# Optimization experiments

Hardware: AMD Instinct MI355X
Metric: run time of the kernel (lower is better)

Reference implementation:

```python
import jax, jax.numpy as jnp
import numpy as np

LAMBDA_COORD = 5.0
LAMBDA_NOOBJ = 0.5
EPS = 1e-9


def _bbox_iou(px, py, pr, gx, gy, gr):
    """IoU of the axis-aligned bounding squares of two circles (x, y, r)."""
    l1, r1, t1, b1 = px - pr, px + pr, py - pr, py + pr
    l2, r2, t2, b2 = gx - gr, gx + gr, gy - gr, gy + gr
    iw = jnp.maximum(jnp.minimum(r1, r2) - jnp.maximum(l1, l2), 0.0)
    ih = jnp.maximum(jnp.minimum(b1, b2) - jnp.maximum(t1, t2), 0.0)
    inter = iw * ih
    a1 = (r1 - l1) * (b1 - t1)
    a2 = (r2 - l2) * (b2 - t2)
    return inter / (a1 + a2 - inter + EPS)


def setup_inputs() -> dict:
    key = jax.random.key(0)
    k1, k2, k3, k4 = jax.random.split(key, 4)
    B, L, G, C = 65536, 16, 8, 8
    pred = jax.random.uniform(k1, (B, G, G, C), dtype=jnp.float32)
    label_rc = jax.random.randint(k2, (B, L, 2), 0, G, dtype=jnp.int32)
    xy = jax.random.uniform(k3, (B, L, 2), dtype=jnp.float32)
    r = jax.random.uniform(k4, (B, L, 1), dtype=jnp.float32) * 0.2 + 0.01
    label_box = jnp.concatenate([xy, r], axis=-1)
    return {"pred": pred, "label_rc": label_rc, "label_box": label_box}


def reference(pred, label_rc, label_box):
    B = pred.shape[0]
    rows = label_rc[..., 0]  # [B, L]
    cols = label_rc[..., 1]
    bidx = jnp.arange(B)[:, None]
    pb = pred[bidx, rows, cols]  # [B, L, 8] responsible cell per label

    gx, gy, gr = label_box[..., 0], label_box[..., 1], label_box[..., 2]
    iou1 = _bbox_iou(pb[..., 0], pb[..., 1], pb[..., 2], gx, gy, gr)
    iou2 = _bbox_iou(pb[..., 4], pb[..., 5], pb[..., 6], gx, gy, gr)

    swap = iou2 > iou1
    cx = jnp.where(swap, pb[..., 4], pb[..., 0])
    cy = jnp.where(swap, pb[..., 5], pb[..., 1])
    cr = jnp.where(swap, pb[..., 6], pb[..., 2])
    conf = jnp.where(swap, pb[..., 7], pb[..., 3])
    un_conf = jnp.where(swap, pb[..., 3], pb[..., 7])
    bigger = jnp.where(swap, iou2, iou1)
    smaller = jnp.where(swap, iou1, iou2)

    coord_loss = LAMBDA_COORD * jnp.sum(
        (cx - gx) ** 2 + (cy - gy) ** 2 + (cr - gr) ** 2)
    cond_loss = jnp.sum((bigger - conf) ** 2)
    cond_loss = cond_loss + LAMBDA_NOOBJ * jnp.sum((smaller - un_conf) ** 2)

    # object mask over the 8x8 grid (duplicates collapse to 1, as in original)
    obj_mask = jnp.zeros(pred.shape[:3], dtype=pred.dtype).at[bidx, rows, cols].set(1.0)
    noobj = (pred[..., 3] ** 2 + pred[..., 7] ** 2) * (1.0 - obj_mask)
    cond_loss = cond_loss + LAMBDA_NOOBJ * jnp.sum(noobj)

    return (coord_loss + cond_loss) / B
```

## Files before the change

kernel.cpp:

```cpp
#include <hip/hip_runtime.h>


static constexpr float LAMBDA_COORD = 5.0f;
static constexpr float LAMBDA_NOOBJ = 0.5f;
static constexpr float EPS_F = 1e-9f;

__device__ __forceinline__ float bbox_iou(float px, float py, float pr,
                                          float gx, float gy, float gr) {
    float l1 = px - pr, r1 = px + pr, t1 = py - pr, b1 = py + pr;
    float l2 = gx - gr, r2 = gx + gr, t2 = gy - gr, b2 = gy + gr;
    float iw = fmaxf(fminf(r1, r2) - fmaxf(l1, l2), 0.0f);
    float ih = fmaxf(fminf(b1, b2) - fmaxf(t1, t2), 0.0f);
    float inter = iw * ih;
    float a1 = (r1 - l1) * (b1 - t1);
    float a2 = (r2 - l2) * (b2 - t2);
    return inter / (a1 + a2 - inter + EPS_F);
}

__global__ void zero_out_kernel(float* __restrict__ out) { *out = 0.0f; }

__global__ __launch_bounds__(256) void yolo_loss_kernel(
    const float* __restrict__ pred,
    const int*   __restrict__ label_rc,
    const float* __restrict__ label_box,
    float* __restrict__ out,
    int B, int L, float invB)
{
    const int lane    = threadIdx.x & 63;
    const int wave_ib = threadIdx.x >> 6;
    const int wave    = blockIdx.x * (blockDim.x >> 6) + wave_ib;
    const int nwaves  = gridDim.x * (blockDim.x >> 6);

    float acc = 0.0f;

    for (int b = wave; b < B; b += nwaves) {
        const float* cell_ptr = pred + ((size_t)b << 9) + ((size_t)lane << 3);
        float4 q0 = *(const float4*)(cell_ptr);
        float4 q1 = *(const float4*)(cell_ptr + 4);

        int   cell = -1;
        float gx = 0.f, gy = 0.f, gr = 0.f;
        if (lane < L) {
            const int2 rc = *(const int2*)(label_rc + ((size_t)b * L + lane) * 2);
            cell = rc.x * 8 + rc.y;
            const float* lb = label_box + ((size_t)b * L + lane) * 3;
            gx = lb[0]; gy = lb[1]; gr = lb[2];
        }

        bool labeled = false;
        #pragma unroll
        for (int l = 0; l < 16; ++l) {
            if (l < L) labeled |= (__shfl(cell, l) == lane);
        }

        int src = (cell < 0) ? 0 : cell;
        float p0 = __shfl(q0.x, src);
        float p1 = __shfl(q0.y, src);
        float p2 = __shfl(q0.z, src);
        float p3 = __shfl(q0.w, src);
        float p4 = __shfl(q1.x, src);
        float p5 = __shfl(q1.y, src);
        float p6 = __shfl(q1.z, src);
        float p7 = __shfl(q1.w, src);

        float contrib = labeled ? 0.0f
                      : LAMBDA_NOOBJ * (q0.w * q0.w + q1.w * q1.w);

        if (lane < L) {
            float iou1 = bbox_iou(p0, p1, p2, gx, gy, gr);
            float iou2 = bbox_iou(p4, p5, p6, gx, gy, gr);
            bool  sw   = iou2 > iou1;
            float cx      = sw ? p4 : p0;
            float cy      = sw ? p5 : p1;
            float cr      = sw ? p6 : p2;
            float conf    = sw ? p7 : p3;
            float un_conf = sw ? p3 : p7;
            float bigger  = sw ? iou2 : iou1;
            float smaller = sw ? iou1 : iou2;
            float dx = cx - gx, dy = cy - gy, dr = cr - gr;
            contrib += LAMBDA_COORD * (dx * dx + dy * dy + dr * dr);
            float d1 = bigger - conf;
            float d2 = smaller - un_conf;
            contrib += d1 * d1 + LAMBDA_NOOBJ * (d2 * d2);
        }

        acc += contrib;
    }

    #pragma unroll
    for (int off = 32; off > 0; off >>= 1)
        acc += __shfl_xor(acc, off);

    __shared__ float wsum[4];
    if (lane == 0) wsum[wave_ib] = acc;
    __syncthreads();
    if (threadIdx.x == 0) {
        float s = wsum[0] + wsum[1] + wsum[2] + wsum[3];
        atomicAdd(out, s * invB);
    }
}

extern "C" void kernel_launch(void* const* d_in, const int* in_sizes, int n_in,
                              void* d_out, int out_size, void* d_ws, size_t ws_size,
                              hipStream_t stream) {
    const float* pred      = (const float*)d_in[0];
    const int*   label_rc  = (const int*)d_in[1];
    const float* label_box = (const float*)d_in[2];
    float*       out       = (float*)d_out;

    const int B = in_sizes[0] / 512;
    const int L = in_sizes[1] / (B * 2);
    const float invB = 1.0f / (float)B;

    zero_out_kernel<<<1, 1, 0, stream>>>(out);

    const int threads = 256;
    const int blocks  = 1024;
    yolo_loss_kernel<<<blocks, threads, 0, stream>>>(
        pred, label_rc, label_box, out, B, L, invB);
}
```

Before: 210.3 us.

## Launch one wave per batch item and replace atomics with two-pass reduction

```diff
diff --git a/kernel.cpp b/kernel.cpp
--- a/kernel.cpp
+++ b/kernel.cpp
@@ -17,23 +17,20 @@
     return inter / (a1 + a2 - inter + EPS_F);
 }
 
-__global__ void zero_out_kernel(float* __restrict__ out) { *out = 0.0f; }
-
 __global__ __launch_bounds__(256) void yolo_loss_kernel(
     const float* __restrict__ pred,
     const int*   __restrict__ label_rc,
     const float* __restrict__ label_box,
-    float* __restrict__ out,
-    int B, int L, float invB)
+    float* __restrict__ partials,
+    int B, int L)
 {
     const int lane    = threadIdx.x & 63;
     const int wave_ib = threadIdx.x >> 6;
-    const int wave    = blockIdx.x * (blockDim.x >> 6) + wave_ib;
-    const int nwaves  = gridDim.x * (blockDim.x >> 6);
+    const int b       = blockIdx.x * 4 + wave_ib;
 
-    float acc = 0.0f;
+    float contrib = 0.0f;
 
-    for (int b = wave; b < B; b += nwaves) {
+    if (b < B) {
         const float* cell_ptr = pred + ((size_t)b << 9) + ((size_t)lane << 3);
         float4 q0 = *(const float4*)(cell_ptr);
         float4 q1 = *(const float4*)(cell_ptr + 4);
@@ -63,8 +60,8 @@
         float p6 = __shfl(q1.z, src);
         float p7 = __shfl(q1.w, src);
 
-        float contrib = labeled ? 0.0f
-                      : LAMBDA_NOOBJ * (q0.w * q0.w + q1.w * q1.w);
+        contrib = labeled ? 0.0f
+                : LAMBDA_NOOBJ * (q0.w * q0.w + q1.w * q1.w);
 
         if (lane < L) {
             float iou1 = bbox_iou(p0, p1, p2, gx, gy, gr);
@@ -83,21 +80,40 @@
             float d2 = smaller - un_conf;
             contrib += d1 * d1 + LAMBDA_NOOBJ * (d2 * d2);
         }
-
-        acc += contrib;
     }
 
     #pragma unroll
     for (int off = 32; off > 0; off >>= 1)
-        acc += __shfl_xor(acc, off);
+        contrib += __shfl_xor(contrib, off);
 
     __shared__ float wsum[4];
-    if (lane == 0) wsum[wave_ib] = acc;
+    if (lane == 0) wsum[wave_ib] = contrib;
     __syncthreads();
-    if (threadIdx.x == 0) {
-        float s = wsum[0] + wsum[1] + wsum[2] + wsum[3];
-        atomicAdd(out, s * invB);
+    if (threadIdx.x == 0)
+        partials[blockIdx.x] = wsum[0] + wsum[1] + wsum[2] + wsum[3];
+}
+
+__global__ __launch_bounds__(256) void reduce_kernel(
+    const float* __restrict__ partials, float* __restrict__ out,
+    int n4, float invB)
+{
+    const float4* p4 = (const float4*)partials;
+    float4 s4 = make_float4(0.f, 0.f, 0.f, 0.f);
+    for (int i = threadIdx.x; i < n4; i += 256) {
+        float4 v = p4[i];
+        s4.x += v.x; s4.y += v.y; s4.z += v.z; s4.w += v.w;
     }
+    float s = (s4.x + s4.y) + (s4.z + s4.w);
+    #pragma unroll
+    for (int off = 32; off > 0; off >>= 1)
+        s += __shfl_xor(s, off);
+
+    __shared__ float wsum[4];
+    const int lane = threadIdx.x & 63, w = threadIdx.x >> 6;
+    if (lane == 0) wsum[w] = s;
+    __syncthreads();
+    if (threadIdx.x == 0)
+        out[0] = (wsum[0] + wsum[1] + wsum[2] + wsum[3]) * invB;
 }
 
 extern "C" void kernel_launch(void* const* d_in, const int* in_sizes, int n_in,
@@ -107,15 +123,15 @@
     const int*   label_rc  = (const int*)d_in[1];
     const float* label_box = (const float*)d_in[2];
     float*       out       = (float*)d_out;
+    float*       partials  = (float*)d_ws;
 
     const int B = in_sizes[0] / 512;
     const int L = in_sizes[1] / (B * 2);
     const float invB = 1.0f / (float)B;
 
-    zero_out_kernel<<<1, 1, 0, stream>>>(out);
+    const int blocks = (B + 3) / 4;
+    yolo_loss_kernel<<<blocks, 256, 0, stream>>>(
+        pred, label_rc, label_box, partials, B, L);
 
-    const int threads = 256;
-    const int blocks  = 1024;
-    yolo_loss_kernel<<<blocks, threads, 0, stream>>>(
-        pred, label_rc, label_box, out, B, L, invB);
+    reduce_kernel<<<1, 256, 0, stream>>>(partials, out, blocks / 4, invB);
 }
```

Result: no change. 207.8 us (-1.2%).
